# Performance work log

Measured on AMD Instinct MI355X. Metric: run time of the kernel, lower is better.

Reference implementation:

```python
import jax, jax.numpy as jnp
import numpy as np

B, NS, NT, C = 32, 1000, 100, 256
LAMBDA_GIOU, LAMBDA_L1 = 10.0, 1.0


def _lsa(cost):
    """Hungarian / Jonker-Volgenant shortest-augmenting-path (numpy, O(n^2 m)).
    Matches scipy.optimize.linear_sum_assignment for rectangular matrices."""
    cost = np.asarray(cost, dtype=np.float64)
    transposed = cost.shape[0] > cost.shape[1]
    if transposed:
        cost = cost.T
    n, m = cost.shape  # n <= m
    INF = np.inf
    u = np.zeros(n + 1)
    v = np.zeros(m + 1)
    p = np.zeros(m + 1, dtype=np.int64)   # p[j] = row (1-based) assigned to col j
    way = np.zeros(m + 1, dtype=np.int64)
    for i in range(1, n + 1):
        p[0] = i
        j0 = 0
        minv = np.full(m + 1, INF)
        used = np.zeros(m + 1, dtype=bool)
        while True:
            used[j0] = True
            i0 = p[j0]
            cur = cost[i0 - 1, :] - u[i0] - v[1:]
            free = ~used[1:]
            better = free & (cur < minv[1:])
            minv[1:][better] = cur[better]
            way[1:][better] = j0
            masked = np.where(free, minv[1:], INF)
            j1 = int(np.argmin(masked)) + 1
            delta = masked[j1 - 1]
            u[p[used]] += delta
            v[used] -= delta
            minv[~used] -= delta
            j0 = j1
            if p[j0] == 0:
                break
        while j0:
            j1 = way[j0]
            p[j0] = p[j1]
            j0 = j1
    rows = p[1:] - 1
    cols = np.arange(m)
    keep = rows >= 0
    rows, cols = rows[keep], cols[keep]
    if transposed:
        rows, cols = cols, rows
    order = np.argsort(rows)
    return rows[order], cols[order]


def _pairwise_cost(logits, classes, sb, tb):
    """Per-batch (Ns,Nt) cost = CE(logits_s, class_t) + 10*(1-GIoU(box_s, box_t)) + L1mean."""
    Bc, Ns, Cd = logits.shape
    Nt = classes.shape[1]
    # Cross entropy: logsumexp over classes minus logit at target class (identical
    # math to the torch expand+flatten CE, without the Ns*Nt*C copy).
    lse = jax.nn.logsumexp(logits, axis=-1)  # (B,Ns)
    picked = jnp.take_along_axis(
        logits, jnp.broadcast_to(classes[:, None, :], (Bc, Ns, Nt)), axis=2)  # (B,Ns,Nt)
    ce = lse[:, :, None] - picked
    # Pairwise GIoU (boxes in xyxy)
    s = sb[:, :, None, :]  # (B,Ns,1,4)
    t = tb[:, None, :, :]  # (B,1,Nt,4)
    ix1 = jnp.maximum(s[..., 0], t[..., 0])
    iy1 = jnp.maximum(s[..., 1], t[..., 1])
    ix2 = jnp.minimum(s[..., 2], t[..., 2])
    iy2 = jnp.minimum(s[..., 3], t[..., 3])
    inter = jnp.clip(ix2 - ix1, 0.0) * jnp.clip(iy2 - iy1, 0.0)
    area_s = (s[..., 2] - s[..., 0]) * (s[..., 3] - s[..., 1])
    area_t = (t[..., 2] - t[..., 0]) * (t[..., 3] - t[..., 1])
    union = area_s + area_t - inter
    iou = inter / union
    cx1 = jnp.minimum(s[..., 0], t[..., 0])
    cy1 = jnp.minimum(s[..., 1], t[..., 1])
    cx2 = jnp.maximum(s[..., 2], t[..., 2])
    cy2 = jnp.maximum(s[..., 3], t[..., 3])
    carea = (cx2 - cx1) * (cy2 - cy1)
    giou = iou - (carea - union) / carea
    l1 = jnp.abs(s - t).mean(axis=-1)  # (B,Ns,Nt)
    return ce + LAMBDA_GIOU * (1.0 - giou) + LAMBDA_L1 * l1


def _valid_boxes(key, b, n):
    p = jax.random.uniform(key, (b, n, 2, 2), dtype=jnp.float32)
    lo = p.min(axis=2)
    hi = p.max(axis=2)
    return jnp.concatenate([lo, hi], axis=-1)  # (b,n,4) xyxy, x1<x2, y1<y2


def setup_inputs() -> dict:
    key = jax.random.key(0)
    k1, k2, k3, k4 = jax.random.split(key, 4)
    return {
        "source_class_logits": jax.random.normal(k1, (B, NS, C), dtype=jnp.float32),
        "target_classes": jax.random.randint(k2, (B, NT), 0, C, dtype=jnp.int32),
        "source_boxes": _valid_boxes(k3, B, NS),
        "target_boxes": _valid_boxes(k4, B, NT),
    }


def reference(source_class_logits, target_classes, source_boxes, target_boxes):
    cost = _pairwise_cost(source_class_logits, target_classes, source_boxes, target_boxes)
    cost_np = np.asarray(cost)
    rows_l, cols_l = [], []
    for b in range(cost_np.shape[0]):  # assignment is inherently per-matrix / host-side
        r, c = _lsa(cost_np[b])
        rows_l.append(r)
        cols_l.append(c)
    rows = jnp.asarray(np.stack(rows_l))  # (B, min(Ns,Nt))
    cols = jnp.asarray(np.stack(cols_l))
    bidx = jnp.arange(cost.shape[0])[:, None]
    return cost[bidx, rows, cols].mean(axis=1)  # (B,)
```

## Files before the change

### kernel.cpp

```cpp
#include <hip/hip_runtime.h>
#include <math.h>

#define NSRC 1000
#define NTGT 100
#define NCLS 256
#define NB   32
#define NSP  1024
#define PAD_IDX(j) ((j) + ((j) >> 4))
#define LDSN (NSP + (NSP >> 4))
#define AUCTION_EPS 0.01f
#define NWAVES 8
#define ROUND_CAP 160


__global__ __launch_bounds__(256) void lse_kernel(const float* __restrict__ logits,
                                                  float* __restrict__ lse) {
    int wid  = threadIdx.x >> 6;
    int lane = threadIdx.x & 63;
    int row0 = blockIdx.x * 32 + wid * 8;
    #pragma unroll 2
    for (int r = 0; r < 8; ++r) {
        int row = row0 + r;
        float4 v4 = reinterpret_cast<const float4*>(logits + (size_t)row * NCLS)[lane];
        float m = fmaxf(fmaxf(v4.x, v4.y), fmaxf(v4.z, v4.w));
        #pragma unroll
        for (int off = 32; off >= 1; off >>= 1) m = fmaxf(m, __shfl_xor(m, off));
        float s = expf(v4.x - m) + expf(v4.y - m) + expf(v4.z - m) + expf(v4.w - m);
        #pragma unroll
        for (int off = 32; off >= 1; off >>= 1) s += __shfl_xor(s, off);
        if (lane == 0) lse[row] = m + logf(s);
    }
}

__global__ __launch_bounds__(256) void cost_kernel(const float* __restrict__ logits,
                                                   const int*   __restrict__ tcls,
                                                   const float* __restrict__ sbox,
                                                   const float* __restrict__ tbox,
                                                   const float* __restrict__ lse,
                                                   float*       __restrict__ cost,
                                                   float*       __restrict__ urow_g,
                                                   int*         __restrict__ jmin_g,
                                                   float*       __restrict__ m2_g) {
    int b  = blockIdx.x & 31;
    int t  = blockIdx.x >> 5;
    int bt = b * NTGT + t;
    int cls = tcls[bt];
    float4 tb = reinterpret_cast<const float4*>(tbox)[bt];
    float area_t = (tb.z - tb.x) * (tb.w - tb.y);
    float* crow = cost + (size_t)bt * NSP;
    float m1 = 1e38f, m2 = 1e38f; int mi = 0x7fffffff;
    for (int s = threadIdx.x; s < NSP; s += 256) {
        if (s >= NSRC) { crow[s] = 1e30f; continue; }
        int gs = b * NSRC + s;
        float4 sb = reinterpret_cast<const float4*>(sbox)[gs];
        float ce = lse[gs] - logits[(size_t)gs * NCLS + cls];
        float ix1 = fmaxf(sb.x, tb.x), iy1 = fmaxf(sb.y, tb.y);
        float ix2 = fminf(sb.z, tb.z), iy2 = fminf(sb.w, tb.w);
        float inter = fmaxf(ix2 - ix1, 0.f) * fmaxf(iy2 - iy1, 0.f);
        float area_s = (sb.z - sb.x) * (sb.w - sb.y);
        float uni = area_s + area_t - inter;
        float iou = inter / uni;
        float cx1 = fminf(sb.x, tb.x), cy1 = fminf(sb.y, tb.y);
        float cx2 = fmaxf(sb.z, tb.z), cy2 = fmaxf(sb.w, tb.w);
        float carea = (cx2 - cx1) * (cy2 - cy1);
        float giou = iou - (carea - uni) / carea;
        float l1 = 0.25f * (fabsf(sb.x - tb.x) + fabsf(sb.y - tb.y) +
                            fabsf(sb.z - tb.z) + fabsf(sb.w - tb.w));
        float c = ce + 10.0f * (1.0f - giou) + l1;
        crow[s] = c;
        if (c < m1) { m2 = m1; m1 = c; mi = s; }
        else if (c < m2) m2 = c;
    }
    #pragma unroll
    for (int off = 32; off >= 1; off >>= 1) {
        float om1 = __shfl_xor(m1, off);
        float om2 = __shfl_xor(m2, off);
        int   oi  = __shfl_xor(mi, off);
        bool take = (om1 < m1) || (om1 == m1 && oi < mi);
        float lose = take ? m1 : om1;
        m1 = take ? om1 : m1;
        mi = take ? oi  : mi;
        m2 = fminf(fminf(m2, om2), lose);
    }
    __shared__ float smin[4], smin2[4];
    __shared__ int   sidx[4];
    int wid = threadIdx.x >> 6, lane = threadIdx.x & 63;
    if (lane == 0) { smin[wid] = m1; smin2[wid] = m2; sidx[wid] = mi; }
    __syncthreads();
    if (threadIdx.x == 0) {
        #pragma unroll
        for (int w = 1; w < 4; ++w) {
            float om1 = smin[w], om2 = smin2[w]; int oi = sidx[w];
            bool take = (om1 < m1) || (om1 == m1 && oi < mi);
            float lose = take ? m1 : om1;
            m1 = take ? om1 : m1;
            mi = take ? oi  : mi;
            m2 = fminf(fminf(m2, om2), lose);
        }
        urow_g[bt] = m1;
        jmin_g[bt] = mi;
        m2_g[bt]   = m2;
    }
}

__global__ __launch_bounds__(512) void lsa_kernel(const float* __restrict__ cost,
                                                  const float* __restrict__ urow_g,
                                                  const int*   __restrict__ jmin_g,
                                                  const float* __restrict__ m2_g,
                                                  float* __restrict__ out) {
    int b    = blockIdx.x;
    int tid  = threadIdx.x;
    int wv   = tid >> 6;
    int lane = tid & 63;
    const float* C = cost + (size_t)b * NTGT * NSP;
    __shared__ int   way[LDSN];
    __shared__ int   pcol[LDSN];
    __shared__ float uu[LDSN];
    __shared__ float vsh[LDSN];
    __shared__ float urow[NTGT];
    __shared__ int   done[NTGT];
    __shared__ float bm1[NTGT];
    __shared__ float bm2[NTGT];
    __shared__ int   bj [NTGT];
    __shared__ float bv [NTGT];
    __shared__ int   qbuf[1024];
    __shared__ int   qstate[2];
    __shared__ int   srow[NWAVES];

    for (int t = tid; t < LDSN; t += 512) {
        pcol[t] = -1; uu[t] = 0.f; vsh[t] = 0.f; way[t] = 0x7fffffff;
    }
    for (int t = tid; t < NTGT; t += 512) {
        float m1 = urow_g[b * NTGT + t];
        urow[t] = m1;
        bm1[t]  = m1;
        bm2[t]  = m2_g[b * NTGT + t];
        bj[t]   = jmin_g[b * NTGT + t];
        bv[t]   = 0.f;
    }
    if (tid == 0) { qstate[0] = 0; qstate[1] = 0; }
    __syncthreads();

    for (int r = tid; r < NTGT; r += 512) atomicMin(&way[PAD_IDX(bj[r])], r);
    __syncthreads();
    for (int r = tid; r < NTGT; r += 512) {
        int j = bj[r];
        int w = (way[PAD_IDX(j)] == r) ? 1 : 0;
        done[r] = w;
        if (w) { pcol[PAD_IDX(j)] = r; uu[PAD_IDX(j)] = urow[r]; }
    }
    __syncthreads();

    if (tid < 64) {
        int qt = 0;
        #pragma unroll
        for (int r0 = 0; r0 < 128; r0 += 64) {
            int r = r0 + lane;
            bool act = (r < NTGT) && !done[r];
            unsigned long long mask = __ballot(act);
            if (act) qbuf[qt + __popcll(mask & ((1ull << lane) - 1ull))] = r;
            qt += __popcll(mask);
        }
        if (lane == 0) qstate[1] = qt;
    }
    __syncthreads();

    int base = lane * 16;

    for (int round = 0; round < ROUND_CAP; ++round) {
        int qh = qstate[0], qt = qstate[1];
        int navail = qt - qh;
        if (navail <= 0) break;
        int take = navail < NWAVES ? navail : NWAVES;
        if (wv < take) {
            int i = qbuf[(qh + wv) & 1023];
            if (lane == 0) srow[wv] = i;
            float m1p = bm1[i] + (bv[i] - vsh[PAD_IDX(bj[i])]);
            if (m1p > bm2[i]) {
                const float4* row4 = reinterpret_cast<const float4*>(C + (size_t)i * NSP + base);
                float m1 = 1e38f, m2 = 1e38f; int j1 = 0x7fffffff;
                #pragma unroll
                for (int q = 0; q < 4; ++q) {
                    float4 c4 = row4[q];
                    float vals[4];
                    vals[0] = c4.x - vsh[PAD_IDX(base + 4*q + 0)];
                    vals[1] = c4.y - vsh[PAD_IDX(base + 4*q + 1)];
                    vals[2] = c4.z - vsh[PAD_IDX(base + 4*q + 2)];
                    vals[3] = c4.w - vsh[PAD_IDX(base + 4*q + 3)];
                    #pragma unroll
                    for (int e = 0; e < 4; ++e) {
                        float val = vals[e];
                        if (val < m1) { m2 = m1; m1 = val; j1 = base + 4*q + e; }
                        else m2 = fminf(m2, val);
                    }
                }
                #pragma unroll
                for (int off = 32; off >= 1; off >>= 1) {
                    float om1 = __shfl_xor(m1, off);
                    float om2 = __shfl_xor(m2, off);
                    int   oj1 = __shfl_xor(j1, off);
                    bool tk = (om1 < m1) || (om1 == m1 && oj1 < j1);
                    float lose = tk ? m1 : om1;
                    m1 = tk ? om1 : m1;
                    j1 = tk ? oj1 : j1;
                    m2 = fminf(fminf(m2, om2), lose);
                }
                if (lane == 0) {
                    bm1[i] = m1; bm2[i] = m2; bj[i] = j1;
                    bv[i]  = vsh[PAD_IDX(j1)];
                }
            }
        }
        __syncthreads();
        if (tid == 0) {
            int qt2 = qstate[1];
            for (int s = 0; s < take; ++s) {
                int i  = srow[s];
                int j1 = bj[i];
                int pj1 = PAD_IDX(j1);
                float vnow = vsh[pj1];
                float m1p  = bm1[i] + (bv[i] - vnow);
                if (m1p <= bm2[i]) {
                    float delta = fmaxf(bm2[i] - m1p, AUCTION_EPS);
                    int old = pcol[pj1];
                    vsh[pj1]  = vnow - delta;
                    pcol[pj1] = i;
                    uu[pj1]   = m1p + delta;
                    urow[i]   = m1p + delta;
                    done[i]   = 1;
                    if (old >= 0) { qbuf[qt2 & 1023] = old; ++qt2; done[old] = 0; }
                } else {
                    qbuf[qt2 & 1023] = i; ++qt2;
                }
            }
            qstate[0] = qstate[0] + take;
            qstate[1] = qt2;
        }
        __syncthreads();
    }

    float v[16], d[16];
    if (tid < 64) {
        #pragma unroll
        for (int k = 0; k < 16; ++k) v[k] = vsh[PAD_IDX(base + k)];
    }
    __syncthreads();

    for (int i = 0; i < NTGT; ++i) {
        if (done[i]) continue;
        float ui = urow[i];
        float Df = 0.f;
        int jf = -1;
        if (tid < 64) {
            const float4* row4 = reinterpret_cast<const float4*>(C + (size_t)i * NSP + base);
            #pragma unroll
            for (int q = 0; q < 4; ++q) {
                float4 c4 = row4[q];
                d[4*q+0] = c4.x - ui - v[4*q+0];
                d[4*q+1] = c4.y - ui - v[4*q+1];
                d[4*q+2] = c4.z - ui - v[4*q+2];
                d[4*q+3] = c4.w - ui - v[4*q+3];
            }
            #pragma unroll
            for (int k = 0; k < 16; ++k) way[PAD_IDX(base + k)] = -1;
            unsigned int used = 0;

            for (int it = 0; it < NTGT + 3; ++it) {
                float lmin = 1e38f;
                #pragma unroll
                for (int k = 0; k < 16; ++k) {
                    float val = ((used >> k) & 1u) ? 1e38f : d[k];
                    lmin = fminf(lmin, val);
                }
                float wmin = lmin;
                #pragma unroll
                for (int off = 32; off >= 1; off >>= 1) wmin = fminf(wmin, __shfl_xor(wmin, off));
                unsigned long long msk = __ballot(lmin == wmin);
                int src = __ffsll(msk) - 1;
                int myk = -1;
                #pragma unroll
                for (int k = 15; k >= 0; --k)
                    if (!((used >> k) & 1u) && d[k] == wmin) myk = k;
                int j0 = __shfl(base + myk, src);
                if (j0 < 0) break;
                int pj0 = pcol[PAD_IDX(j0)];
                if (pj0 < 0) { Df = wmin; jf = j0; break; }
                if ((j0 >> 4) == lane) used |= 1u << (j0 & 15);
                float uref = uu[PAD_IDX(j0)];
                float sft  = wmin - uref;
                const float4* rr = reinterpret_cast<const float4*>(C + (size_t)pj0 * NSP + base);
                float cr[16];
                #pragma unroll
                for (int q = 0; q < 4; ++q) {
                    float4 c4 = rr[q];
                    cr[4*q+0] = c4.x; cr[4*q+1] = c4.y; cr[4*q+2] = c4.z; cr[4*q+3] = c4.w;
                }
                #pragma unroll
                for (int k = 0; k < 16; ++k) {
                    float cand = sft + cr[k] - v[k];
                    bool upd = (cand < d[k]) && !((used >> k) & 1u);
                    if (upd) { d[k] = cand; way[PAD_IDX(base + k)] = j0; }
                }
            }

            if (jf >= 0) {
                #pragma unroll
                for (int k = 0; k < 16; ++k) {
                    if ((used >> k) & 1u) {
                        float diff = Df - d[k];
                        v[k] -= diff;
                        uu[PAD_IDX(base + k)] += diff;
                    }
                }
            }
        }
        __syncthreads();
        if (tid == 0 && jf >= 0) {
            int j = jf;
            for (int g = 0; g < NSP; ++g) {
                int jp = way[PAD_IDX(j)];
                if (jp < 0) { pcol[PAD_IDX(j)] = i; uu[PAD_IDX(j)] = ui + Df; break; }
                pcol[PAD_IDX(j)] = pcol[PAD_IDX(jp)];
                uu[PAD_IDX(j)]   = uu[PAD_IDX(jp)];
                j = jp;
            }
            done[i] = 1;
        }
        __syncthreads();
    }

    if (tid < 64) {
        float acc = 0.f;
        #pragma unroll
        for (int k = 0; k < 16; ++k) {
            int j = base + k;
            if (j < NSRC) {
                int r = pcol[PAD_IDX(j)];
                if (r >= 0) acc += C[(size_t)r * NSP + j];
            }
        }
        #pragma unroll
        for (int off = 32; off >= 1; off >>= 1) acc += __shfl_xor(acc, off);
        if (lane == 0) out[b] = acc * (1.0f / NTGT);
    }
}

extern "C" void kernel_launch(void* const* d_in, const int* in_sizes, int n_in,
                              void* d_out, int out_size, void* d_ws, size_t ws_size,
                              hipStream_t stream) {
    const float* logits = (const float*)d_in[0];
    const int*   tcls   = (const int*)  d_in[1];
    const float* sbox   = (const float*)d_in[2];
    const float* tbox   = (const float*)d_in[3];
    float* out = (float*)d_out;

    float* lse    = (float*)d_ws;
    float* cost   = lse + 32768;
    float* urow_g = cost + (size_t)NB * NTGT * NSP;
    int*   jmin_g = (int*)(urow_g + NB * NTGT);
    float* m2_g   = (float*)(jmin_g + NB * NTGT);

    lse_kernel <<<1000,      256, 0, stream>>>(logits, lse);
    cost_kernel<<<NB * NTGT, 256, 0, stream>>>(logits, tcls, sbox, tbox, lse, cost,
                                               urow_g, jmin_g, m2_g);
    lsa_kernel <<<NB,        512, 0, stream>>>(cost, urow_g, jmin_g, m2_g, out);
}
```

Before: 127.8 us.

## Prefetch runner-up column's cost row in Dijkstra search; loosen auction epsilon

The shortest-augmenting-path inner loop now tracks the two smallest reduced costs with a top-2 wave reduction and prefetches the cost row of the second-best column's assigned row. If that column is picked next iteration, the global load is replaced by the registers already filled. The auction epsilon is raised and the round cap lowered so the auction phase does fewer, coarser rounds and leaves more work to the exact augmentation. The price is a heavier reduction with more shuffles, extra register pressure, and prefetches that are wasted when the guess is wrong.

Result: no change. 126.8 us (median of 2 runs) (-0.8%).

```diff
diff --git a/kernel.cpp b/kernel.cpp
--- a/kernel.cpp
+++ b/kernel.cpp
@@ -8,9 +8,9 @@
 #define NSP  1024
 #define PAD_IDX(j) ((j) + ((j) >> 4))
 #define LDSN (NSP + (NSP >> 4))
-#define AUCTION_EPS 0.01f
+#define AUCTION_EPS 0.04f
 #define NWAVES 8
-#define ROUND_CAP 160
+#define ROUND_CAP 96
 
 
 __global__ __launch_bounds__(256) void lse_kernel(const float* __restrict__ logits,
@@ -264,36 +264,63 @@
             #pragma unroll
             for (int k = 0; k < 16; ++k) way[PAD_IDX(base + k)] = -1;
             unsigned int used = 0;
+            int   pf_j = -1;
+            float pfr[16];
 
             for (int it = 0; it < NTGT + 3; ++it) {
-                float lmin = 1e38f;
+                float l1 = 1e38f, l2 = 1e38f;
+                int   i1 = 0x7fffffff, i2 = 0x7fffffff;
                 #pragma unroll
                 for (int k = 0; k < 16; ++k) {
                     float val = ((used >> k) & 1u) ? 1e38f : d[k];
-                    lmin = fminf(lmin, val);
-                }
-                float wmin = lmin;
-                #pragma unroll
-                for (int off = 32; off >= 1; off >>= 1) wmin = fminf(wmin, __shfl_xor(wmin, off));
-                unsigned long long msk = __ballot(lmin == wmin);
-                int src = __ffsll(msk) - 1;
-                int myk = -1;
-                #pragma unroll
-                for (int k = 15; k >= 0; --k)
-                    if (!((used >> k) & 1u) && d[k] == wmin) myk = k;
-                int j0 = __shfl(base + myk, src);
-                if (j0 < 0) break;
+                    int idx = base + k;
+                    if (val < l1) { l2 = l1; i2 = i1; l1 = val; i1 = idx; }
+                    else if (val < l2) { l2 = val; i2 = idx; }
+                }
+                #pragma unroll
+                for (int off = 32; off >= 1; off >>= 1) {
+                    float ob1 = __shfl_xor(l1, off), ob2 = __shfl_xor(l2, off);
+                    int   oc1 = __shfl_xor(i1, off), oc2 = __shfl_xor(i2, off);
+                    bool tk = (ob1 < l1) || (ob1 == l1 && oc1 < i1);
+                    float n1 = tk ? ob1 : l1; int ni1 = tk ? oc1 : i1;
+                    float lz = tk ? l1  : ob1; int liz = tk ? i1  : oc1;
+                    float n2 = lz; int ni2 = liz;
+                    if (l2  < n2) { n2 = l2;  ni2 = i2;  }
+                    if (ob2 < n2) { n2 = ob2; ni2 = oc2; }
+                    l1 = n1; i1 = ni1; l2 = n2; i2 = ni2;
+                }
+                float wmin = l1; int j0 = i1; int j0b = i2;
+                if (wmin >= 1e37f) break;
                 int pj0 = pcol[PAD_IDX(j0)];
                 if (pj0 < 0) { Df = wmin; jf = j0; break; }
                 if ((j0 >> 4) == lane) used |= 1u << (j0 & 15);
                 float uref = uu[PAD_IDX(j0)];
                 float sft  = wmin - uref;
-                const float4* rr = reinterpret_cast<const float4*>(C + (size_t)pj0 * NSP + base);
                 float cr[16];
-                #pragma unroll
-                for (int q = 0; q < 4; ++q) {
-                    float4 c4 = rr[q];
-                    cr[4*q+0] = c4.x; cr[4*q+1] = c4.y; cr[4*q+2] = c4.z; cr[4*q+3] = c4.w;
+                if (pf_j == j0) {
+                    #pragma unroll
+                    for (int k = 0; k < 16; ++k) cr[k] = pfr[k];
+                    pf_j = -1;
+                } else {
+                    const float4* rr = reinterpret_cast<const float4*>(C + (size_t)pj0 * NSP + base);
+                    #pragma unroll
+                    for (int q = 0; q < 4; ++q) {
+                        float4 c4 = rr[q];
+                        cr[4*q+0] = c4.x; cr[4*q+1] = c4.y; cr[4*q+2] = c4.z; cr[4*q+3] = c4.w;
+                    }
+                }
+                if (j0b < NSP && j0b != pf_j) {
+                    int pj0b = pcol[PAD_IDX(j0b)];
+                    if (pj0b >= 0) {
+                        const float4* rb = reinterpret_cast<const float4*>(C + (size_t)pj0b * NSP + base);
+                        #pragma unroll
+                        for (int q = 0; q < 4; ++q) {
+                            float4 c4 = rb[q];
+                            pfr[4*q+0] = c4.x; pfr[4*q+1] = c4.y;
+                            pfr[4*q+2] = c4.z; pfr[4*q+3] = c4.w;
+                        }
+                        pf_j = j0b;
+                    } else pf_j = -1;
                 }
                 #pragma unroll
                 for (int k = 0; k < 16; ++k) {
```
